# Kernel tuning notes

Measured on AMD Instinct MI355X. Metric: run time of the kernel, lower is better.

The kernel has to match this reference:

```python
import jax, jax.numpy as jnp
import numpy as np

EPS = 1e-3          # local-max suppression threshold (self.eps)
R = 4               # cost sampling radius around each disparity seed
SPLIT = 4           # stripe width for windowed propagation attention
NH = 4              # prop_n_heads
NUM_PROPOSALS = 4

def _conv1d(x, w, b):
    # x: [N, Cin, D], w: [Cout, Cin, 5], padding=2 (SAME)
    y = jax.lax.conv_general_dilated(x, w, (1,), [(2, 2)], dimension_numbers=('NCH', 'OIH', 'NCH'))
    return y + b[None, :, None]

def _conv2d(x, w, pad):
    return jax.lax.conv_general_dilated(x, w, (1, 1), [(pad, pad), (pad, pad)], dimension_numbers=('NCHW', 'OIHW', 'NCHW'))

def _ln(x, g, b):
    mu = x.mean(-1, keepdims=True)
    var = x.var(-1, keepdims=True)
    return (x - mu) * jax.lax.rsqrt(var + 1e-5) * g + b

def _forward(cost_volume, fmap1, mlp_w1, mlp_b1, mlp_w2, mlp_b2, mlp_w3, mlp_b3,
             proj_w1, proj_w2, embed_w, embed_b, ctx_w, ctx_b,
             ln1_g, ln1_b, qkv_w, qkv_b, attn_w, attn_b, ln2_g, ln2_b,
             fc1_w, fc1_b, fc2_w, fc2_b, normf_g, normf_b,
             h1_w, h1_b, h2_w, h2_b, h3_w, h3_b):
    B, G, D, H, W = cost_volume.shape
    P = NUM_PROPOSALS
    N = B * H * W
    # [B,G,D,H,W] -> [B*H*W, G, D]
    cv = cost_volume.transpose(0, 3, 4, 1, 2).reshape(N, G, D)
    # tiny conv1d cost filter: G -> 8 -> 16 -> 1 channels over disparity dim
    h = jax.nn.relu(_conv1d(cv, mlp_w1, mlp_b1))
    h = jax.nn.relu(_conv1d(h, mlp_w2, mlp_b2))
    cost = _conv1d(h, mlp_w3, mlp_b3)[:, 0, :]                      # [N, D]
    prob = jax.nn.softmax(cost, axis=-1)                             # [N, D]
    # max_pool1d(k=3, s=1, p=1) based local-maxima detection
    pad = jnp.pad(prob, ((0, 0), (1, 1)), constant_values=-jnp.inf)
    pooled = jnp.maximum(jnp.maximum(pad[:, :-2], pad[:, 1:-1]), pad[:, 2:])
    non_local_max = (prob != pooled) & (prob > EPS)
    prob_ = jnp.where(non_local_max, EPS, jax.lax.stop_gradient(prob))
    _, seeds = jax.lax.top_k(prob_, P)                               # [N, P] int32
    # context projection: Conv3x3 (no bias) -> InstanceNorm (affine-free) -> ReLU -> Conv1x1
    c = _conv2d(fmap1, proj_w1, 1)
    mu = c.mean((2, 3), keepdims=True)
    var = c.var((2, 3), keepdims=True)
    c = jax.nn.relu((c - mu) * jax.lax.rsqrt(var + 1e-5))
    ctx = _conv2d(c, proj_w2, 0).transpose(0, 2, 3, 1).reshape(N, -1)  # [N, CTX]
    # seed embedding: gather cost values in a +/-R window around each seed disparity
    offs = jnp.arange(-R, R + 1)
    idx = jnp.clip(seeds[:, :, None] + offs[None, None, :], 0, D - 1)  # [N,P,T]
    feat = jnp.take_along_axis(cv[:, None], idx[:, :, None, :], axis=3)  # [N,P,G,T]
    x = feat.reshape(N, P, -1) @ embed_w + embed_b + (ctx @ ctx_w + ctx_b)[:, None]
    C = x.shape[-1]
    dh = C // NH
    scale = 1.0 / np.sqrt(dh).astype(np.float32)
    nw = W // SPLIT
    x = x.reshape(B, H, nw, SPLIT * P, C)                            # stripe windows
    L = qkv_w.shape[0]
    for l in range(L):
        qkv = x @ qkv_w[l] + qkv_b[l]
        q, k, v = jnp.split(qkv, 3, axis=-1)
        shp = q.shape[:-1]
        q = q.reshape(*shp, NH, dh)
        k = k.reshape(*shp, NH, dh)
        v = v.reshape(*shp, NH, dh)
        att = jnp.einsum('bhwqnd,bhwknd->bhwnqk', q, k) * scale
        att = jax.nn.softmax(att, axis=-1)
        o = jnp.einsum('bhwnqk,bhwknd->bhwqnd', att, v).reshape(*shp, C)
        x = _ln(x + o @ attn_w[l] + attn_b[l], ln1_g[l], ln1_b[l])   # post-norm
        y = jax.nn.gelu(x @ fc1_w[l] + fc1_b[l], approximate=False) @ fc2_w[l] + fc2_b[l]
        x = _ln(x + y, ln2_g[l], ln2_b[l])
    mem = _ln(x, normf_g, normf_b).reshape(N, P, C)
    # prop head: 3-layer MLP -> scalar refinement per proposal
    o = jax.nn.relu(mem @ h1_w + h1_b)
    o = jax.nn.relu(o @ h2_w + h2_b)
    outputs = (o @ h3_w + h3_b)[..., 0][None]                        # [1, N, P]
    labels = jax.nn.relu(outputs + seeds.astype(jnp.float32)[None])  # [1, N, P]
    return cv, prob, seeds, labels

def setup_inputs():
    key = jax.random.key(0)
    ks = iter(jax.random.split(key, 40))
    B, G, D, H, W = 2, 8, 128, 80, 160
    FD, CTX, C, L = 128, 64, 128, 2
    T = 2 * R + 1
    def nrm(shape, scale):
        return jax.random.normal(next(ks), shape, jnp.float32) * scale
    return dict(
        cost_volume=jax.random.normal(next(ks), (B, G, D, H, W), jnp.float32),
        fmap1=jax.random.normal(next(ks), (B, FD, H, W), jnp.float32),
        mlp_w1=nrm((8, G, 5), (2.0 / (G * 5)) ** 0.5), mlp_b1=jnp.zeros((8,), jnp.float32),
        mlp_w2=nrm((16, 8, 5), (2.0 / 40.0) ** 0.5), mlp_b2=jnp.zeros((16,), jnp.float32),
        mlp_w3=nrm((1, 16, 5), (2.0 / 80.0) ** 0.5), mlp_b3=jnp.zeros((1,), jnp.float32),
        proj_w1=nrm((128, FD, 3, 3), (2.0 / (FD * 9)) ** 0.5),
        proj_w2=nrm((CTX, 128, 1, 1), (2.0 / 128.0) ** 0.5),
        embed_w=nrm((G * T, C), 0.02), embed_b=jnp.zeros((C,), jnp.float32),
        ctx_w=nrm((CTX, C), 0.02), ctx_b=jnp.zeros((C,), jnp.float32),
        ln1_g=jnp.ones((L, C), jnp.float32), ln1_b=jnp.zeros((L, C), jnp.float32),
        qkv_w=nrm((L, C, 3 * C), 0.02), qkv_b=jnp.zeros((L, 3 * C), jnp.float32),
        attn_w=nrm((L, C, C), 0.02), attn_b=jnp.zeros((L, C), jnp.float32),
        ln2_g=jnp.ones((L, C), jnp.float32), ln2_b=jnp.zeros((L, C), jnp.float32),
        fc1_w=nrm((L, C, 4 * C), 0.02), fc1_b=jnp.zeros((L, 4 * C), jnp.float32),
        fc2_w=nrm((L, 4 * C, C), 0.02), fc2_b=jnp.zeros((L, C), jnp.float32),
        normf_g=jnp.ones((C,), jnp.float32), normf_b=jnp.zeros((C,), jnp.float32),
        h1_w=nrm((C, C), 0.02), h1_b=jnp.zeros((C,), jnp.float32),
        h2_w=nrm((C, C), 0.02), h2_b=jnp.zeros((C,), jnp.float32),
        h3_w=nrm((C, 1), 0.02), h3_b=jnp.zeros((1,), jnp.float32),
    )

def reference(cost_volume, fmap1, mlp_w1, mlp_b1, mlp_w2, mlp_b2, mlp_w3, mlp_b3,
              proj_w1, proj_w2, embed_w, embed_b, ctx_w, ctx_b,
              ln1_g, ln1_b, qkv_w, qkv_b, attn_w, attn_b, ln2_g, ln2_b,
              fc1_w, fc1_b, fc2_w, fc2_b, normf_g, normf_b,
              h1_w, h1_b, h2_w, h2_b, h3_w, h3_b):
    return _forward(cost_volume, fmap1, mlp_w1, mlp_b1, mlp_w2, mlp_b2, mlp_w3, mlp_b3,
                    proj_w1, proj_w2, embed_w, embed_b, ctx_w, ctx_b,
                    ln1_g, ln1_b, qkv_w, qkv_b, attn_w, attn_b, ln2_g, ln2_b,
                    fc1_w, fc1_b, fc2_w, fc2_b, normf_g, normf_b,
                    h1_w, h1_b, h2_w, h2_b, h3_w, h3_b)
```

## Files before the change

kernel.cpp:

```cpp
#include <hip/hip_runtime.h>
#include <hip/hip_bf16.h>
#include <math.h>

#define B_   2
#define G_   8
#define D_   128
#define H_   80
#define W_   160
#define N_   (B_*H_*W_)
#define P_   4
#define CTX_ 64
#define C_   128
#define FD_  128
#define NROWS (N_*P_)

#define OUT_CV     ((size_t)0)
#define OUT_PROB   ((size_t)26214400)
#define OUT_SEEDS  ((size_t)29491200)
#define OUT_LABELS ((size_t)29593600)

typedef __attribute__((ext_vector_type(8))) short short8;
typedef __attribute__((ext_vector_type(4))) float float4v;

__device__ __forceinline__ float bf2f(unsigned short u){
  unsigned v = ((unsigned)u) << 16;
  return __builtin_bit_cast(float, v);
}
__device__ __forceinline__ unsigned short f2bf(float f){
  __hip_bfloat16 h = __float2bfloat16(f);
  return __builtin_bit_cast(unsigned short, h);
}
__device__ __forceinline__ void load8f(const unsigned short* p, float* f){
  uint4 u = *(const uint4*)p;
  const unsigned short* us = (const unsigned short*)&u;
  #pragma unroll
  for(int i=0;i<8;i++) f[i]=bf2f(us[i]);
}
__device__ __forceinline__ void add_resid32(float* v, const unsigned short* rp){
  #pragma unroll
  for(int i=0;i<4;i++){
    uint4 u = ((const uint4*)rp)[i];
    const unsigned short* us=(const unsigned short*)&u;
    #pragma unroll
    for(int k=0;k<8;k++) v[i*8+k]+=bf2f(us[k]);
  }
}
__device__ __forceinline__ void ln_write32(float* v, int colbase, const float* g, const float* b,
                                           unsigned short* dst){
  float s=0.f, sq=0.f;
  #pragma unroll
  for(int i=0;i<32;i++){ s+=v[i]; sq+=v[i]*v[i]; }
  s  += __shfl_xor(s,1);  sq += __shfl_xor(sq,1);
  s  += __shfl_xor(s,2);  sq += __shfl_xor(sq,2);
  float mu  = s*(1.f/128.f);
  float var = sq*(1.f/128.f) - mu*mu;
  float rs  = rsqrtf(var+1e-5f);
  union{unsigned short us[32]; uint4 u4[4];} pk;
  #pragma unroll
  for(int i=0;i<32;i++) pk.us[i]=f2bf((v[i]-mu)*rs*g[colbase+i]+b[colbase+i]);
  uint4* op=(uint4*)dst;
  #pragma unroll
  for(int i=0;i<4;i++) op[i]=pk.u4[i];
}

struct CvtSeg { const float* src; unsigned short* dst; int ks; int N; int base; };
struct CvtArgs { CvtSeg s[10]; };
__global__ __launch_bounds__(256) void k_cvt_all(CvtArgs a, int grand_total){
  int i = blockIdx.x*256 + threadIdx.x;
  if(i >= grand_total) return;
  int seg = 0;
  #pragma unroll
  for(int s=1;s<10;s++) if(i >= a.s[s].base) seg = s;
  int r = i - a.s[seg].base;
  int ks = a.s[seg].ks;
  int k = r & ((1<<ks)-1);
  int n = r >> ks;
  a.s[seg].dst[r] = f2bf(a.s[seg].src[(size_t)k*a.s[seg].N + n]);
}

__global__ __launch_bounds__(256) void k_cvtW3(const float* __restrict__ w,
                                               unsigned short* __restrict__ BT){
  int i = blockIdx.x*256 + threadIdx.x;
  if(i < 128*1152){
    int co = i / 1152, rem = i % 1152;
    int tap = rem >> 7, ci = rem & 127;
    BT[i] = f2bf(w[((size_t)co*128 + ci)*9 + tap]);
  }
}

__global__ __launch_bounds__(256) void k_fmapT(const float* __restrict__ fmap,
                                               unsigned short* __restrict__ fT){
  __shared__ float t[32][33];
  int w0 = blockIdx.x*32, c0 = blockIdx.y*32;
  int z = blockIdx.z; int b = z / H_; int h = z % H_;
  int tx = threadIdx.x, ty = threadIdx.y;
  #pragma unroll
  for(int i=0;i<4;i++){
    int c = c0 + ty + i*8;
    t[ty+i*8][tx] = fmap[(((size_t)b*FD_ + c)*H_ + h)*W_ + w0 + tx];
  }
  __syncthreads();
  #pragma unroll
  for(int i=0;i<4;i++){
    int wl = ty + i*8;
    fT[(((size_t)b*H_ + h)*W_ + w0 + wl)*128 + c0 + tx] = f2bf(t[tx][wl]);
  }
}

__global__ __launch_bounds__(256) void k_transpose(const float* __restrict__ cvol,
                                                   float* __restrict__ outf){
  __shared__ float t[32][33];
  int z = blockIdx.z;
  int h = z % H_;  int bg = z / H_;
  int w0 = blockIdx.x*32, d0 = blockIdx.y*32;
  int tx = threadIdx.x, ty = threadIdx.y;
  #pragma unroll
  for(int i=0;i<4;i++){
    int d = d0 + ty + i*8;
    t[ty+i*8][tx] = cvol[(((size_t)bg*D_ + d)*H_ + h)*W_ + w0 + tx];
  }
  __syncthreads();
  int b = bg / G_, g = bg % G_;
  #pragma unroll
  for(int i=0;i<4;i++){
    int wl = ty + i*8;
    int n = (b*H_+h)*W_ + w0 + wl;
    size_t o = ((size_t)n*G_ + g)*D_ + d0 + tx;
    outf[OUT_CV + o] = t[tx][wl];
  }
}

__global__ __launch_bounds__(128) void k_cost(
    const float* __restrict__ w1, const float* __restrict__ b1,
    const float* __restrict__ w2, const float* __restrict__ b2,
    const float* __restrict__ w3, const float* __restrict__ b3,
    float* __restrict__ outf, int* __restrict__ seeds_i){
  __shared__ float cvs[G_][D_];
  __shared__ float h1s[8][D_];
  __shared__ float h2s[16][D_];
  __shared__ float ps[D_];
  __shared__ float pv[D_];
  __shared__ float rv[D_];
  __shared__ int   ri[D_];
  __shared__ float red[D_];
  int n = blockIdx.x, d = threadIdx.x;
  const float* cvf = outf + OUT_CV;
  #pragma unroll
  for(int g=0; g<G_; g++) cvs[g][d] = cvf[((size_t)n*G_+g)*D_ + d];
  __syncthreads();
  float a1[8];
  #pragma unroll
  for(int c=0;c<8;c++) a1[c]=b1[c];
  for(int g=0; g<8; g++)
    #pragma unroll
    for(int j=0;j<5;j++){
      int idx = d + j - 2;
      float v = (idx>=0 && idx<D_) ? cvs[g][idx] : 0.f;
      #pragma unroll
      for(int c=0;c<8;c++) a1[c] += v * w1[(c*8+g)*5 + j];
    }
  #pragma unroll
  for(int c=0;c<8;c++) h1s[c][d]=fmaxf(a1[c],0.f);
  __syncthreads();
  float a2[16];
  #pragma unroll
  for(int c=0;c<16;c++) a2[c]=b2[c];
  for(int g=0; g<8; g++)
    #pragma unroll
    for(int j=0;j<5;j++){
      int idx = d + j - 2;
      float v = (idx>=0 && idx<D_) ? h1s[g][idx] : 0.f;
      #pragma unroll
      for(int c=0;c<16;c++) a2[c] += v * w2[(c*8+g)*5 + j];
    }
  #pragma unroll
  for(int c=0;c<16;c++) h2s[c][d]=fmaxf(a2[c],0.f);
  __syncthreads();
  float cost=b3[0];
  for(int g=0; g<16; g++)
    #pragma unroll
    for(int j=0;j<5;j++){
      int idx = d + j - 2;
      if(idx>=0 && idx<D_) cost += h2s[g][idx]*w3[g*5+j];
    }
  red[d]=cost; __syncthreads();
  for(int s=64;s>0;s>>=1){ if(d<s) red[d]=fmaxf(red[d],red[d+s]); __syncthreads(); }
  float m=red[0]; __syncthreads();
  float e=expf(cost-m);
  red[d]=e; __syncthreads();
  for(int s=64;s>0;s>>=1){ if(d<s) red[d]+=red[d+s]; __syncthreads(); }
  float prob = e/red[0];
  ps[d]=prob;
  outf[OUT_PROB + (size_t)n*D_ + d] = prob;
  __syncthreads();
  float pooled = prob;
  if(d>0)    pooled = fmaxf(pooled, ps[d-1]);
  if(d<127)  pooled = fmaxf(pooled, ps[d+1]);
  bool nlm = (prob != pooled) && (prob > 1e-3f);
  pv[d] = nlm ? 1e-3f : prob;
  __syncthreads();
  for(int p=0;p<P_;p++){
    rv[d]=pv[d]; ri[d]=d; __syncthreads();
    for(int s=64;s>0;s>>=1){
      if(d<s){
        float vb=rv[d+s]; int ib=ri[d+s];
        if(vb>rv[d] || (vb==rv[d] && ib<ri[d])){ rv[d]=vb; ri[d]=ib; }
      }
      __syncthreads();
    }
    if(d==0){
      int sd = ri[0];
      seeds_i[n*P_+p]=sd;
      outf[OUT_SEEDS + (size_t)n*P_ + p]=(float)sd;
      pv[sd] = -1e30f;
    }
    __syncthreads();
  }
}

__global__ __launch_bounds__(256) void k_conv3(const unsigned short* __restrict__ fT,
                                               const unsigned short* __restrict__ BT,
                                               float* __restrict__ tmp3){
  __shared__ __align__(16) unsigned short hal[4*34*136];
  int t = threadIdx.x, lane = t & 63, wv = t >> 6;
  int m = lane & 15, q = lane >> 4;
  int w0 = blockIdx.x*32;
  int h0 = blockIdx.y*2;
  int bz = blockIdx.z;
  int b  = bz >> 1;
  int co0 = (bz & 1)*64;
  for(int idx=t; idx<4*34*16; idx+=256){
    int chunk = idx & 15;
    int pos = idx >> 4;
    int r = pos / 34, wl = pos % 34;
    int gh = h0 - 1 + r, gw = w0 - 1 + wl;
    uint4 v = {0u,0u,0u,0u};
    if(gh>=0 && gh<H_ && gw>=0 && gw<W_)
      v = *(const uint4*)(fT + ((((size_t)b*H_+gh)*W_+gw)<<7) + chunk*8);
    *(uint4*)&hal[pos*136 + chunk*8] = v;
  }
  __syncthreads();
  int rowt = wv >> 1, wcol = (wv & 1)*16;
  float4v acc[4];
  #pragma unroll
  for(int i=0;i<4;i++) acc[i]=(float4v){0.f,0.f,0.f,0.f};
  #pragma unroll
  for(int ky=0;ky<3;ky++){
    #pragma unroll
    for(int kx=0;kx<3;kx++){
      int tap = ky*3+kx;
      const unsigned short* abase = &hal[((rowt+ky)*34 + wcol + m + kx)*136 + q*8];
      short8 af[4];
      #pragma unroll
      for(int kk=0;kk<4;kk++) af[kk] = *(const short8*)(abase + kk*32);
      #pragma unroll
      for(int nt=0;nt<4;nt++){
        const short8* bp = (const short8*)(BT + (size_t)(co0 + nt*16 + m)*1152 + tap*128);
        #pragma unroll
        for(int kk=0;kk<4;kk++)
          acc[nt] = __builtin_amdgcn_mfma_f32_16x16x32_bf16(af[kk], bp[kk*4+q], acc[nt], 0,0,0);
      }
    }
  }
  int h = h0 + rowt;
  #pragma unroll
  for(int nt=0;nt<4;nt++){
    int co = co0 + nt*16 + m;
    *(float4v*)(tmp3 + (((size_t)b*128+co)*H_ + h)*W_ + w0 + wcol + q*4) = acc[nt];
  }
}

__global__ __launch_bounds__(256) void k_inorm(const float* __restrict__ tmp3,
                                               float* __restrict__ musg){
  int bc = blockIdx.x;
  const float* p = tmp3 + (size_t)bc*H_*W_;
  float s=0.f, sq=0.f;
  for(int i=threadIdx.x;i<H_*W_;i+=256){ float v=p[i]; s+=v; sq+=v*v; }
  __shared__ float rs_[256], rq_[256];
  rs_[threadIdx.x]=s; rq_[threadIdx.x]=sq; __syncthreads();
  for(int st=128;st>0;st>>=1){
    if(threadIdx.x<st){ rs_[threadIdx.x]+=rs_[threadIdx.x+st]; rq_[threadIdx.x]+=rq_[threadIdx.x+st]; }
    __syncthreads();
  }
  if(threadIdx.x==0){
    float mu = rs_[0]/(float)(H_*W_);
    float var = rq_[0]/(float)(H_*W_) - mu*mu;
    musg[bc*2]=mu; musg[bc*2+1]=rsqrtf(var+1e-5f);
  }
}

__global__ __launch_bounds__(256) void k_ctx(const float* __restrict__ tmp3,
                                             const float* __restrict__ musg,
                                             const float* __restrict__ w2,
                                             float* __restrict__ ctxT){
  __shared__ float nl[128][33];
  int w0 = blockIdx.x*32; int h = blockIdx.y; int b = blockIdx.z;
  int t = threadIdx.x;
  for(int idx=t; idx<128*32; idx+=256){
    int c = idx>>5, wl = idx&31;
    float v = tmp3[(((size_t)b*128+c)*H_+h)*W_+w0+wl];
    v = (v - musg[(b*128+c)*2]) * musg[(b*128+c)*2+1];
    nl[c][wl] = fmaxf(v, 0.f);
  }
  __syncthreads();
  int wl = t & 31, cg = t >> 5;
  float acc[8]={0.f,0.f,0.f,0.f,0.f,0.f,0.f,0.f};
  for(int c=0;c<128;c++){
    float v = nl[c][wl];
    #pragma unroll
    for(int j=0;j<8;j++) acc[j] += v * w2[(size_t)(cg*8+j)*128 + c];
  }
  int n = (b*H_+h)*W_ + w0 + wl;
  #pragma unroll
  for(int j=0;j<8;j++) ctxT[(size_t)(cg*8+j)*N_ + n] = acc[j];
}

__global__ __launch_bounds__(256) void k_embed(const float* __restrict__ outf,
    const float* __restrict__ ctxT, const int* __restrict__ seeds_i,
    const float* __restrict__ embed_w, const float* __restrict__ embed_b,
    const float* __restrict__ ctx_w, const float* __restrict__ ctx_b,
    unsigned short* __restrict__ Xb){
  __shared__ float feats[16][72];
  __shared__ float cvv[4][64];
  const float* cvf = outf + OUT_CV;
  int n0 = blockIdx.x*4;
  int t = threadIdx.x;
  for(int idx=t; idx<16*72; idx+=256){
    int r = idx/72, j = idx%72;
    int n = n0 + (r>>2), p = r&3;
    int sd = seeds_i[n*4+p];
    int g = j/9, tt = j%9;
    int di = sd + tt - 4; di = di<0?0:(di>127?127:di);
    feats[r][j] = cvf[((size_t)n*8+g)*128 + di];
  }
  for(int idx=t; idx<4*64; idx+=256){
    int nl_ = idx>>6, k = idx&63;
    cvv[nl_][k] = ctxT[(size_t)k*N_ + n0+nl_];
  }
  __syncthreads();
  int col = t & 127, rg = t >> 7;
  float acc[8];
  float bb = embed_b[col] + ctx_b[col];
  #pragma unroll
  for(int r=0;r<8;r++) acc[r]=bb;
  for(int j=0;j<72;j++){
    float wv = embed_w[(size_t)j*128+col];
    #pragma unroll
    for(int r=0;r<8;r++) acc[r] += feats[rg*8+r][j]*wv;
  }
  for(int k=0;k<64;k++){
    float wv = ctx_w[(size_t)k*128+col];
    #pragma unroll
    for(int r=0;r<8;r++) acc[r] += cvv[(rg*8+r)>>2][k]*wv;
  }
  #pragma unroll
  for(int r=0;r<8;r++){
    int row = n0*4 + rg*8 + r;
    Xb[(size_t)row*128 + col] = f2bf(acc[r]);
  }
}

__global__ __launch_bounds__(256) void k_qkv_attn(const unsigned short* __restrict__ Xb,
    const unsigned short* __restrict__ qkvT, const float* __restrict__ qkv_b,
    unsigned short* __restrict__ Ob){
  __shared__ __align__(16) unsigned short qb[64][136];
  __shared__ __align__(16) unsigned short kb[64][136];
  __shared__ __align__(16) unsigned short vb[64][136];
  int t = threadIdx.x, lane = t & 63, wv = t >> 6;
  int m = lane & 15, q = lane >> 4;
  int rbase = blockIdx.x*64;
  int row = rbase + wv*16 + m;
  short8 af[4];
  const short8* ap = (const short8*)(Xb + (size_t)row*128);
  #pragma unroll
  for(int kk=0;kk<4;kk++) af[kk] = ap[kk*4+q];
  for(int nt=0; nt<24; nt++){
    int n0 = nt*16;
    float4v acc = {0.f,0.f,0.f,0.f};
    const short8* bp = (const short8*)(qkvT + (size_t)(n0 + m)*128);
    #pragma unroll
    for(int kk=0;kk<4;kk++)
      acc = __builtin_amdgcn_mfma_f32_16x16x32_bf16(af[kk], bp[kk*4+q], acc, 0,0,0);
    int col = n0 + m;
    float bias = qkv_b[col];
    unsigned short* dst = (col<128)? &qb[0][0] : (col<256? &kb[0][0] : &vb[0][0]);
    int cl = col & 127;
    #pragma unroll
    for(int j=0;j<4;j++){
      int rr = wv*16 + q*4 + j;
      dst[rr*136 + cl] = f2bf(acc[j] + bias);
    }
  }
  __syncthreads();
  int win = t >> 6, head = (t>>4)&3, qr = t & 15;
  const float scale = 0.17677669529663687f;
  float qv[32];
  load8f(&qb[win*16+qr][head*32+0],  qv+0);
  load8f(&qb[win*16+qr][head*32+8],  qv+8);
  load8f(&qb[win*16+qr][head*32+16], qv+16);
  load8f(&qb[win*16+qr][head*32+24], qv+24);
  float s[16];
  #pragma unroll
  for(int k=0;k<16;k++){
    float kvv[32];
    load8f(&kb[win*16+k][head*32+0],  kvv+0);
    load8f(&kb[win*16+k][head*32+8],  kvv+8);
    load8f(&kb[win*16+k][head*32+16], kvv+16);
    load8f(&kb[win*16+k][head*32+24], kvv+24);
    float a=0.f;
    #pragma unroll
    for(int d=0;d<32;d++) a += qv[d]*kvv[d];
    s[k]=a*scale;
  }
  float mx=s[0];
  #pragma unroll
  for(int k=1;k<16;k++) mx=fmaxf(mx,s[k]);
  float sum=0.f;
  #pragma unroll
  for(int k=0;k<16;k++){ s[k]=__expf(s[k]-mx); sum+=s[k]; }
  float inv=1.f/sum;
  float o[32];
  #pragma unroll
  for(int d=0;d<32;d++) o[d]=0.f;
  #pragma unroll
  for(int k=0;k<16;k++){
    float p = s[k]*inv;
    float vvv[32];
    load8f(&vb[win*16+k][head*32+0],  vvv+0);
    load8f(&vb[win*16+k][head*32+8],  vvv+8);
    load8f(&vb[win*16+k][head*32+16], vvv+16);
    load8f(&vb[win*16+k][head*32+24], vvv+24);
    #pragma unroll
    for(int d=0;d<32;d++) o[d] += p*vvv[d];
  }
  union{unsigned short us[32]; uint4 u4[4];} pk;
  #pragma unroll
  for(int d=0;d<32;d++) pk.us[d]=f2bf(o[d]);
  uint4* op=(uint4*)(Ob + (size_t)(rbase + win*16 + qr)*128 + head*32);
  #pragma unroll
  for(int i=0;i<4;i++) op[i]=pk.u4[i];
}

template<int MODE>
__global__ __launch_bounds__(256) void k_gemm128(const unsigned short* __restrict__ Ab,
    const unsigned short* __restrict__ WT, const float* __restrict__ bias,
    const unsigned short* __restrict__ resid, const float* __restrict__ lng,
    const float* __restrict__ lnb, unsigned short* __restrict__ outb){
  __shared__ float ef[64*132];
  int t=threadIdx.x, lane=t&63, wv=t>>6;
  int m=lane&15, q=lane>>4;
  int rbase=blockIdx.x*64;
  short8 af[4];
  const short8* ap=(const short8*)(Ab + (size_t)(rbase+wv*16+m)*128);
  #pragma unroll
  for(int kk=0;kk<4;kk++) af[kk]=ap[kk*4+q];
  #pragma unroll
  for(int nt=0;nt<8;nt++){
    float4v acc={0.f,0.f,0.f,0.f};
    const short8* bp=(const short8*)(WT + (size_t)(nt*16+m)*128);
    #pragma unroll
    for(int kk=0;kk<4;kk++)
      acc=__builtin_amdgcn_mfma_f32_16x16x32_bf16(af[kk],bp[kk*4+q],acc,0,0,0);
    int col=nt*16+m;
    float bv=bias[col];
    #pragma unroll
    for(int j=0;j<4;j++) ef[(wv*16+q*4+j)*132 + col]=acc[j]+bv;
  }
  __syncthreads();
  int r=t>>2, qq=t&3;
  float v[32];
  const float* er=&ef[r*132+qq*32];
  #pragma unroll
  for(int i=0;i<32;i++) v[i]=er[i];
  size_t gro=(size_t)(rbase+r)*128+qq*32;
  if(MODE==0){
    union{unsigned short us[32]; uint4 u4[4];} pk;
    #pragma unroll
    for(int i=0;i<32;i++) pk.us[i]=f2bf(fmaxf(v[i],0.f));
    uint4* op=(uint4*)(outb+gro);
    #pragma unroll
    for(int i=0;i<4;i++) op[i]=pk.u4[i];
  } else {
    add_resid32(v, resid+gro);
    ln_write32(v, qq*32, lng, lnb, outb+gro);
  }
}

__global__ __launch_bounds__(256) void k_mlp(const unsigned short* __restrict__ X2b,
    const unsigned short* __restrict__ fc1T, const float* __restrict__ fc1b,
    const unsigned short* __restrict__ fc2T, const float* __restrict__ fc2b,
    const float* __restrict__ lng, const float* __restrict__ lnb,
    unsigned short* __restrict__ Xbout){
  __shared__ __align__(16) unsigned short hb[64*512];
  int t=threadIdx.x, lane=t&63, wv=t>>6;
  int m=lane&15, q=lane>>4;
  int rbase=blockIdx.x*64;
  short8 af[4];
  const short8* ap=(const short8*)(X2b + (size_t)(rbase+wv*16+m)*128);
  #pragma unroll
  for(int kk=0;kk<4;kk++) af[kk]=ap[kk*4+q];
  for(int half=0; half<2; half++){
    float4v acc[16];
    #pragma unroll
    for(int i=0;i<16;i++) acc[i]=(float4v){0.f,0.f,0.f,0.f};
    #pragma unroll
    for(int nt=0;nt<16;nt++){
      int n0=(half*16+nt)*16;
      const short8* bp=(const short8*)(fc1T + (size_t)(n0+m)*128);
      #pragma unroll
      for(int kk=0;kk<4;kk++)
        acc[nt]=__builtin_amdgcn_mfma_f32_16x16x32_bf16(af[kk],bp[kk*4+q],acc[nt],0,0,0);
    }
    #pragma unroll
    for(int nt=0;nt<16;nt++){
      int col=(half*16+nt)*16+m;
      float bv=fc1b[col];
      int bblk = col>>3;
      #pragma unroll
      for(int j=0;j<4;j++){
        int rr=wv*16+q*4+j;
        float x=acc[nt][j]+bv;
        float gel = 0.5f*x*(1.f+erff(x*0.70710678118654752f));
        hb[rr*512 + ((bblk ^ (rr&63))<<3) + (col&7)] = f2bf(gel);
      }
    }
  }
  __syncthreads();
  int arow = wv*16+m;
  short8 haf[16];
  #pragma unroll
  for(int kk=0;kk<16;kk++){
    int bb=kk*4+q;
    haf[kk]=*(const short8*)&hb[arow*512 + ((bb ^ (arow&63))<<3)];
  }
  float4v acc2[8];
  #pragma unroll
  for(int i=0;i<8;i++) acc2[i]=(float4v){0.f,0.f,0.f,0.f};
  #pragma unroll
  for(int nt=0;nt<8;nt++){
    const short8* bp=(const short8*)(fc2T + (size_t)(nt*16+m)*512);
    #pragma unroll
    for(int kk=0;kk<16;kk++)
      acc2[nt]=__builtin_amdgcn_mfma_f32_16x16x32_bf16(haf[kk],bp[kk*4+q],acc2[nt],0,0,0);
  }
  __syncthreads();
  float* ef=(float*)hb;
  #pragma unroll
  for(int nt=0;nt<8;nt++){
    int col=nt*16+m;
    float bv=fc2b[col];
    #pragma unroll
    for(int j=0;j<4;j++) ef[(wv*16+q*4+j)*132+col]=acc2[nt][j]+bv;
  }
  __syncthreads();
  int r=t>>2, qq=t&3;
  float v[32];
  #pragma unroll
  for(int i=0;i<32;i++) v[i]=ef[r*132+qq*32+i];
  size_t gro=(size_t)(rbase+r)*128+qq*32;
  add_resid32(v, X2b+gro);
  ln_write32(v, qq*32, lng, lnb, Xbout+gro);
}

__global__ __launch_bounds__(256) void k_lnfinal(const unsigned short* __restrict__ Xb,
    const float* __restrict__ g, const float* __restrict__ b,
    unsigned short* __restrict__ Mb){
  int t=threadIdx.x;
  int r=t>>2, qq=t&3;
  size_t gro=(size_t)(blockIdx.x*64+r)*128+qq*32;
  float v[32];
  #pragma unroll
  for(int i=0;i<4;i++){
    uint4 u=((const uint4*)(Xb+gro))[i];
    const unsigned short* us=(const unsigned short*)&u;
    #pragma unroll
    for(int k=0;k<8;k++) v[i*8+k]=bf2f(us[k]);
  }
  ln_write32(v, qq*32, g, b, Mb+gro);
}

__global__ __launch_bounds__(256) void k_head3(const unsigned short* __restrict__ H2b,
    const float* __restrict__ h3w, const float* __restrict__ h3b,
    const int* __restrict__ seeds_i, float* __restrict__ outf){
  int row=blockIdx.x*256+threadIdx.x;
  const uint4* rp=(const uint4*)(H2b+(size_t)row*128);
  float acc=h3b[0];
  #pragma unroll
  for(int i=0;i<8;i++){
    uint4 u=rp[i];
    const unsigned short* us=(const unsigned short*)&u;
    #pragma unroll
    for(int j=0;j<8;j++) acc += bf2f(us[j])*h3w[i*8+j];
  }
  float lab=fmaxf(acc+(float)seeds_i[row],0.f);
  outf[OUT_LABELS+row]=lab;
}

extern "C" void kernel_launch(void* const* d_in, const int* in_sizes, int n_in,
                              void* d_out, int out_size, void* d_ws, size_t ws_size,
                              hipStream_t stream) {
  const float* cost_volume=(const float*)d_in[0];
  const float* fmap1   =(const float*)d_in[1];
  const float* mlp_w1  =(const float*)d_in[2];
  const float* mlp_b1  =(const float*)d_in[3];
  const float* mlp_w2  =(const float*)d_in[4];
  const float* mlp_b2  =(const float*)d_in[5];
  const float* mlp_w3  =(const float*)d_in[6];
  const float* mlp_b3  =(const float*)d_in[7];
  const float* proj_w1 =(const float*)d_in[8];
  const float* proj_w2 =(const float*)d_in[9];
  const float* embed_w =(const float*)d_in[10];
  const float* embed_b =(const float*)d_in[11];
  const float* ctx_w   =(const float*)d_in[12];
  const float* ctx_b   =(const float*)d_in[13];
  const float* ln1_g   =(const float*)d_in[14];
  const float* ln1_b   =(const float*)d_in[15];
  const float* qkv_w   =(const float*)d_in[16];
  const float* qkv_b   =(const float*)d_in[17];
  const float* attn_w  =(const float*)d_in[18];
  const float* attn_b  =(const float*)d_in[19];
  const float* ln2_g   =(const float*)d_in[20];
  const float* ln2_b   =(const float*)d_in[21];
  const float* fc1_w   =(const float*)d_in[22];
  const float* fc1_b   =(const float*)d_in[23];
  const float* fc2_w   =(const float*)d_in[24];
  const float* fc2_b   =(const float*)d_in[25];
  const float* normf_g =(const float*)d_in[26];
  const float* normf_b =(const float*)d_in[27];
  const float* h1_w    =(const float*)d_in[28];
  const float* h1_b    =(const float*)d_in[29];
  const float* h2_w    =(const float*)d_in[30];
  const float* h2_b    =(const float*)d_in[31];
  const float* h3_w    =(const float*)d_in[32];
  const float* h3_b    =(const float*)d_in[33];
  float* outf = (float*)d_out;

  char* ws=(char*)d_ws;
  unsigned short* act    =(unsigned short*)(ws + 0);
  float*          tmp3   =(float*)(ws + 104857600);
  float*          musg   =(float*)(ws + 117964800);
  float*          ctxT   =(float*)(ws + 117966848);
  int*            seeds_i=(int*)  (ws + 124520448);
  unsigned short* Xb     =(unsigned short*)(ws + 124930048);
  unsigned short* X2b    =(unsigned short*)(ws + 151144448);
  unsigned short* wbf    =(unsigned short*)(ws + 177358848);
  const size_t NEEDED = 178210816;
  if (ws_size < NEEDED) return;
  unsigned short* fT  = act;
  unsigned short* BT3 = act + 3276800;
  unsigned short* Ob  = act;
  unsigned short* Mb  = Ob  + 13107200;
  unsigned short* H1b = Mb  + 13107200;
  unsigned short* H2b = H1b + 13107200;
  unsigned short* qkvT = wbf;
  unsigned short* attnT= wbf + 98304;
  unsigned short* fc1T = wbf + 131072;
  unsigned short* fc2T = wbf + 262144;
  unsigned short* h1T  = wbf + 393216;
  unsigned short* h2T  = wbf + 409600;

  CvtArgs ca;
  int base = 0;
  auto seg=[&](int i,const float* s,unsigned short* d,int ks,int Nn,int cnt){
    ca.s[i].src=s; ca.s[i].dst=d; ca.s[i].ks=ks; ca.s[i].N=Nn; ca.s[i].base=base; base+=cnt;
  };
  seg(0, qkv_w,        qkvT,        7, 384, 49152);
  seg(1, qkv_w+49152,  qkvT+49152,  7, 384, 49152);
  seg(2, attn_w,       attnT,       7, 128, 16384);
  seg(3, attn_w+16384, attnT+16384, 7, 128, 16384);
  seg(4, fc1_w,        fc1T,        7, 512, 65536);
  seg(5, fc1_w+65536,  fc1T+65536,  7, 512, 65536);
  seg(6, fc2_w,        fc2T,        9, 128, 65536);
  seg(7, fc2_w+65536,  fc2T+65536,  9, 128, 65536);
  seg(8, h1_w,         h1T,         7, 128, 16384);
  seg(9, h2_w,         h2T,         7, 128, 16384);
  k_cvt_all<<<(base+255)/256,256,0,stream>>>(ca, base);
  k_cvtW3<<<576,256,0,stream>>>(proj_w1, BT3);
  k_fmapT<<<dim3(5,4,160), dim3(32,8), 0, stream>>>(fmap1, fT);

  k_transpose<<<dim3(5,4,1280), dim3(32,8), 0, stream>>>(cost_volume, outf);
  k_cost<<<N_,128,0,stream>>>(mlp_w1,mlp_b1, mlp_w2,mlp_b2, mlp_w3,mlp_b3, outf, seeds_i);

  k_conv3<<<dim3(5,40,4),256,0,stream>>>(fT, BT3, tmp3);
  k_inorm<<<256,256,0,stream>>>(tmp3, musg);
  k_ctx<<<dim3(5,80,2),256,0,stream>>>(tmp3, musg, proj_w2, ctxT);

  k_embed<<<6400,256,0,stream>>>(outf, ctxT, seeds_i, embed_w, embed_b, ctx_w, ctx_b, Xb);

  for(int l=0;l<2;l++){
    k_qkv_attn<<<1600,256,0,stream>>>(Xb, qkvT + (size_t)l*49152, qkv_b + l*384, Ob);
    k_gemm128<1><<<1600,256,0,stream>>>(Ob, attnT + (size_t)l*16384, attn_b + l*128,
                                        Xb, ln1_g + l*128, ln1_b + l*128, X2b);
    k_mlp<<<1600,256,0,stream>>>(X2b, fc1T + (size_t)l*65536, fc1_b + l*512,
                                 fc2T + (size_t)l*65536, fc2_b + l*128,
                                 ln2_g + l*128, ln2_b + l*128, Xb);
  }

  k_lnfinal<<<1600,256,0,stream>>>(Xb, normf_g, normf_b, Mb);
  k_gemm128<0><<<1600,256,0,stream>>>(Mb,  h1T, h1_b, nullptr, nullptr, nullptr, H1b);
  k_gemm128<0><<<1600,256,0,stream>>>(H1b, h2T, h2_b, nullptr, nullptr, nullptr, H2b);
  k_head3<<<400,256,0,stream>>>(H2b, h3_w, h3_b, seeds_i, outf);
}
```

Measured before the change: 1.750 ms.

## Rewrite cost filter as one wavefront per pixel with shuffle reductions

The cost-filter kernel now maps one 64-lane wavefront to each pixel, four pixels per 256-thread block, with each lane computing two disparities using packed float2 FMAs. The zero-padded shared-memory halo removes the per-tap bounds checks. The block-wide tree reductions for softmax and the iterative top-k argmax, each needing many barriers, become wavefront shuffle reductions. This aims to cut barrier and shared-memory traffic in a kernel launched once per pixel, at the cost of more registers per thread.

```diff
diff --git a/kernel.cpp b/kernel.cpp
--- a/kernel.cpp
+++ b/kernel.cpp
@@ -21,6 +21,7 @@
 
 typedef __attribute__((ext_vector_type(8))) short short8;
 typedef __attribute__((ext_vector_type(4))) float float4v;
+typedef __attribute__((ext_vector_type(2))) float v2f;
 
 __device__ __forceinline__ float bf2f(unsigned short u){
   unsigned v = ((unsigned)u) << 16;
@@ -130,91 +131,123 @@
   }
 }
 
-__global__ __launch_bounds__(128) void k_cost(
+__global__ __launch_bounds__(256) void k_cost(
     const float* __restrict__ w1, const float* __restrict__ b1,
     const float* __restrict__ w2, const float* __restrict__ b2,
     const float* __restrict__ w3, const float* __restrict__ b3,
     float* __restrict__ outf, int* __restrict__ seeds_i){
-  __shared__ float cvs[G_][D_];
-  __shared__ float h1s[8][D_];
-  __shared__ float h2s[16][D_];
-  __shared__ float ps[D_];
-  __shared__ float pv[D_];
-  __shared__ float rv[D_];
-  __shared__ int   ri[D_];
-  __shared__ float red[D_];
-  int n = blockIdx.x, d = threadIdx.x;
-  const float* cvf = outf + OUT_CV;
-  #pragma unroll
-  for(int g=0; g<G_; g++) cvs[g][d] = cvf[((size_t)n*G_+g)*D_ + d];
-  __syncthreads();
-  float a1[8];
-  #pragma unroll
-  for(int c=0;c<8;c++) a1[c]=b1[c];
+  __shared__ float As[4][16*132];
+  __shared__ float Bs[4][8*132];
+  int t = threadIdx.x, wv = t>>6, lane = t&63;
+  int n = blockIdx.x*4 + wv;
+  float* A  = As[wv];
+  float* Bb = Bs[wv];
+  if(lane < 48){
+    int ch = lane>>1, side = lane&1;
+    float* buf = (ch<16)? (A + ch*132) : (Bb + (ch-16)*132);
+    *(v2f*)(buf + (side?130:0)) = (v2f){0.f,0.f};
+  }
+  const float* cvp = outf + OUT_CV + (size_t)n*(G_*D_);
+  #pragma unroll
   for(int g=0; g<8; g++)
-    #pragma unroll
-    for(int j=0;j<5;j++){
-      int idx = d + j - 2;
-      float v = (idx>=0 && idx<D_) ? cvs[g][idx] : 0.f;
-      #pragma unroll
-      for(int c=0;c<8;c++) a1[c] += v * w1[(c*8+g)*5 + j];
+    *(v2f*)(A + g*132 + 2 + 2*lane) = *(const v2f*)(cvp + g*128 + 2*lane);
+  __syncthreads();
+  v2f a1[8];
+  #pragma unroll
+  for(int c=0;c<8;c++) a1[c] = (v2f){b1[c], b1[c]};
+  #pragma unroll
+  for(int g=0; g<8; g++){
+    const float* base = A + g*132 + 2*lane;
+    v2f vm = *(const v2f*)(base);
+    v2f vc = *(const v2f*)(base+2);
+    v2f vp = *(const v2f*)(base+4);
+    v2f tap0=vm, tap1=(v2f){vm.y,vc.x}, tap2=vc, tap3=(v2f){vc.y,vp.x}, tap4=vp;
+    #pragma unroll
+    for(int c=0;c<8;c++){
+      const float* wp = w1 + (c*8+g)*5;
+      a1[c] = __builtin_elementwise_fma(tap0, (v2f){wp[0],wp[0]}, a1[c]);
+      a1[c] = __builtin_elementwise_fma(tap1, (v2f){wp[1],wp[1]}, a1[c]);
+      a1[c] = __builtin_elementwise_fma(tap2, (v2f){wp[2],wp[2]}, a1[c]);
+      a1[c] = __builtin_elementwise_fma(tap3, (v2f){wp[3],wp[3]}, a1[c]);
+      a1[c] = __builtin_elementwise_fma(tap4, (v2f){wp[4],wp[4]}, a1[c]);
     }
-  #pragma unroll
-  for(int c=0;c<8;c++) h1s[c][d]=fmaxf(a1[c],0.f);
-  __syncthreads();
-  float a2[16];
-  #pragma unroll
-  for(int c=0;c<16;c++) a2[c]=b2[c];
-  for(int g=0; g<8; g++)
-    #pragma unroll
-    for(int j=0;j<5;j++){
-      int idx = d + j - 2;
-      float v = (idx>=0 && idx<D_) ? h1s[g][idx] : 0.f;
-      #pragma unroll
-      for(int c=0;c<16;c++) a2[c] += v * w2[(c*8+g)*5 + j];
+  }
+  #pragma unroll
+  for(int c=0;c<8;c++)
+    *(v2f*)(Bb + c*132 + 2 + 2*lane) = (v2f){fmaxf(a1[c].x,0.f), fmaxf(a1[c].y,0.f)};
+  __syncthreads();
+  v2f a2[16];
+  #pragma unroll
+  for(int c=0;c<16;c++) a2[c] = (v2f){b2[c], b2[c]};
+  #pragma unroll
+  for(int g=0; g<8; g++){
+    const float* base = Bb + g*132 + 2*lane;
+    v2f vm = *(const v2f*)(base);
+    v2f vc = *(const v2f*)(base+2);
+    v2f vp = *(const v2f*)(base+4);
+    v2f tap0=vm, tap1=(v2f){vm.y,vc.x}, tap2=vc, tap3=(v2f){vc.y,vp.x}, tap4=vp;
+    #pragma unroll
+    for(int c=0;c<16;c++){
+      const float* wp = w2 + (c*8+g)*5;
+      a2[c] = __builtin_elementwise_fma(tap0, (v2f){wp[0],wp[0]}, a2[c]);
+      a2[c] = __builtin_elementwise_fma(tap1, (v2f){wp[1],wp[1]}, a2[c]);
+      a2[c] = __builtin_elementwise_fma(tap2, (v2f){wp[2],wp[2]}, a2[c]);
+      a2[c] = __builtin_elementwise_fma(tap3, (v2f){wp[3],wp[3]}, a2[c]);
+      a2[c] = __builtin_elementwise_fma(tap4, (v2f){wp[4],wp[4]}, a2[c]);
     }
-  #pragma unroll
-  for(int c=0;c<16;c++) h2s[c][d]=fmaxf(a2[c],0.f);
-  __syncthreads();
-  float cost=b3[0];
-  for(int g=0; g<16; g++)
-    #pragma unroll
-    for(int j=0;j<5;j++){
-      int idx = d + j - 2;
-      if(idx>=0 && idx<D_) cost += h2s[g][idx]*w3[g*5+j];
+  }
+  #pragma unroll
+  for(int c=0;c<16;c++)
+    *(v2f*)(A + c*132 + 2 + 2*lane) = (v2f){fmaxf(a2[c].x,0.f), fmaxf(a2[c].y,0.f)};
+  __syncthreads();
+  v2f cost = (v2f){b3[0], b3[0]};
+  #pragma unroll
+  for(int g=0; g<16; g++){
+    const float* base = A + g*132 + 2*lane;
+    v2f vm = *(const v2f*)(base);
+    v2f vc = *(const v2f*)(base+2);
+    v2f vp = *(const v2f*)(base+4);
+    v2f tap0=vm, tap1=(v2f){vm.y,vc.x}, tap2=vc, tap3=(v2f){vc.y,vp.x}, tap4=vp;
+    const float* wp = w3 + g*5;
+    cost = __builtin_elementwise_fma(tap0, (v2f){wp[0],wp[0]}, cost);
+    cost = __builtin_elementwise_fma(tap1, (v2f){wp[1],wp[1]}, cost);
+    cost = __builtin_elementwise_fma(tap2, (v2f){wp[2],wp[2]}, cost);
+    cost = __builtin_elementwise_fma(tap3, (v2f){wp[3],wp[3]}, cost);
+    cost = __builtin_elementwise_fma(tap4, (v2f){wp[4],wp[4]}, cost);
+  }
+  float mx = fmaxf(cost.x, cost.y);
+  #pragma unroll
+  for(int off=32; off>0; off>>=1) mx = fmaxf(mx, __shfl_xor(mx, off));
+  v2f e = (v2f){expf(cost.x-mx), expf(cost.y-mx)};
+  float sm = e.x + e.y;
+  #pragma unroll
+  for(int off=32; off>0; off>>=1) sm += __shfl_xor(sm, off);
+  float inv = 1.f/sm;
+  v2f prob = (v2f){e.x*inv, e.y*inv};
+  *(v2f*)(outf + OUT_PROB + (size_t)n*D_ + 2*lane) = prob;
+  float pm = __shfl(prob.y, lane-1);  if(lane==0)  pm = -1e30f;
+  float pp = __shfl(prob.x, lane+1);  if(lane==63) pp = -1e30f;
+  float plx = fmaxf(fmaxf(pm, prob.x), prob.y);
+  float ply = fmaxf(fmaxf(prob.x, prob.y), pp);
+  v2f pv;
+  pv.x = ((prob.x != plx) && (prob.x > 1e-3f)) ? 1e-3f : prob.x;
+  pv.y = ((prob.y != ply) && (prob.y > 1e-3f)) ? 1e-3f : prob.y;
+  #pragma unroll
+  for(int p=0; p<P_; p++){
+    float bv; int bi;
+    if(pv.y > pv.x){ bv=pv.y; bi=2*lane+1; } else { bv=pv.x; bi=2*lane; }
+    #pragma unroll
+    for(int off=1; off<64; off<<=1){
+      float ov = __shfl_xor(bv, off);
+      int   oi = __shfl_xor(bi, off);
+      if(ov > bv || (ov == bv && oi < bi)){ bv=ov; bi=oi; }
     }
-  red[d]=cost; __syncthreads();
-  for(int s=64;s>0;s>>=1){ if(d<s) red[d]=fmaxf(red[d],red[d+s]); __syncthreads(); }
-  float m=red[0]; __syncthreads();
-  float e=expf(cost-m);
-  red[d]=e; __syncthreads();
-  for(int s=64;s>0;s>>=1){ if(d<s) red[d]+=red[d+s]; __syncthreads(); }
-  float prob = e/red[0];
-  ps[d]=prob;
-  outf[OUT_PROB + (size_t)n*D_ + d] = prob;
-  __syncthreads();
-  float pooled = prob;
-  if(d>0)    pooled = fmaxf(pooled, ps[d-1]);
-  if(d<127)  pooled = fmaxf(pooled, ps[d+1]);
-  bool nlm = (prob != pooled) && (prob > 1e-3f);
-  pv[d] = nlm ? 1e-3f : prob;
-  __syncthreads();
-  for(int p=0;p<P_;p++){
-    rv[d]=pv[d]; ri[d]=d; __syncthreads();
-    for(int s=64;s>0;s>>=1){
-      if(d<s){
-        float vb=rv[d+s]; int ib=ri[d+s];
-        if(vb>rv[d] || (vb==rv[d] && ib<ri[d])){ rv[d]=vb; ri[d]=ib; }
-      }
-      __syncthreads();
+    if(lane==0){
+      seeds_i[n*P_+p] = bi;
+      outf[OUT_SEEDS + (size_t)n*P_ + p] = (float)bi;
     }
-    if(d==0){
-      int sd = ri[0];
-      seeds_i[n*P_+p]=sd;
-      outf[OUT_SEEDS + (size_t)n*P_ + p]=(float)sd;
-      pv[sd] = -1e30f;
-    }
-    __syncthreads();
+    if(bi == 2*lane)   pv.x = -1e30f;
+    if(bi == 2*lane+1) pv.y = -1e30f;
   }
 }
 
@@ -679,7 +712,7 @@
   k_fmapT<<<dim3(5,4,160), dim3(32,8), 0, stream>>>(fmap1, fT);
 
   k_transpose<<<dim3(5,4,1280), dim3(32,8), 0, stream>>>(cost_volume, outf);
-  k_cost<<<N_,128,0,stream>>>(mlp_w1,mlp_b1, mlp_w2,mlp_b2, mlp_w3,mlp_b3, outf, seeds_i);
+  k_cost<<<6400,256,0,stream>>>(mlp_w1,mlp_b1, mlp_w2,mlp_b2, mlp_w3,mlp_b3, outf, seeds_i);
 
   k_conv3<<<dim3(5,40,4),256,0,stream>>>(fT, BT3, tmp3);
   k_inorm<<<256,256,0,stream>>>(tmp3, musg);
```

After: 1.514 ms. -13.5%, faster.
